# Kernel optimization log

Measured on AMD Instinct MI355X. Metric: run time of the kernel, lower is better.

Reference implementation:

```python
import jax, jax.numpy as jnp
import numpy as np


def _mlp(x, W1, b1, W2, b2):
    # Linear -> exact GELU (torch nn.GELU default) -> Linear
    h = jax.nn.gelu(x @ W1 + b1, approximate=False)
    return h @ W2 + b2


def setup_inputs() -> dict:
    B, L, H, NB, D, HID = 4, 4096, 16, 64, 1024, 128
    NS = H * NB
    key = jax.random.key(0)
    ks = jax.random.split(key, 6)
    theta_path = jax.random.normal(ks[0], (B, L, H, NB), dtype=jnp.float32)
    content_emb = jax.random.normal(ks[1], (B, L, D), dtype=jnp.float32)
    log_Pi = jnp.zeros((H, NB), dtype=jnp.float32)
    s1 = 1.0 / np.sqrt(D)
    s2 = 1.0 / np.sqrt(HID)
    # log_R_head: Linear(D,128) -> GELU -> Linear(128,NS), last weight scaled by 0.01, bias 0
    Wr1 = jax.random.uniform(ks[2], (D, HID), jnp.float32, -s1, s1)
    br1 = jnp.zeros((HID,), jnp.float32)
    Wr2 = jax.random.uniform(ks[3], (HID, NS), jnp.float32, -s2, s2) * 0.01
    br2 = jnp.zeros((NS,), jnp.float32)
    # measure_head: Linear(D,128) -> GELU -> Linear(128,NS)
    Wm1 = jax.random.uniform(ks[4], (D, HID), jnp.float32, -s1, s1)
    bm1 = jnp.zeros((HID,), jnp.float32)
    Wm2 = jax.random.uniform(ks[5], (HID, NS), jnp.float32, -s2, s2)
    bm2 = jnp.zeros((NS,), jnp.float32)
    return {
        "theta_path": theta_path, "content_emb": content_emb, "log_Pi": log_Pi,
        "Wr1": Wr1, "br1": br1, "Wr2": Wr2, "br2": br2,
        "Wm1": Wm1, "bm1": bm1, "Wm2": Wm2, "bm2": bm2,
    }


def reference(theta_path, content_emb, log_Pi, Wr1, br1, Wr2, br2, Wm1, bm1, Wm2, bm2):
    B, L, H, NB = theta_path.shape
    # per-token measurement noise R_t
    log_R = jnp.clip(_mlp(content_emb, Wr1, br1, Wr2, br2).reshape(B, L, H, NB), -5.0, 5.0)
    R = jnp.exp(log_R)
    # measurement z in (-pi, pi)
    z = jnp.pi * jnp.tanh(_mlp(content_emb, Wm1, bm1, Wm2, bm2).reshape(B, L, H, NB))
    diff = z - theta_path
    nu = jnp.arctan2(jnp.sin(diff), jnp.cos(diff))  # wrapped innovation
    Pi = jnp.exp(log_Pi)            # (H, NB) constant covariance
    Pi_b = Pi[None, None]           # (1,1,H,NB)
    K = Pi_b / jnp.maximum(Pi_b + R, 1e-8)  # Kalman gain
    alpha = 1.0 - K
    u = K * nu
    # scalar affine parallel scan: d[t] = alpha[t]*d[t-1] + u[t], d[-1]=0
    def combine(c1, c2):
        a1, v1 = c1
        a2, v2 = c2
        return a1 * a2, a2 * v1 + v2
    _, d = jax.lax.associative_scan(combine, (alpha, u), axis=1)
    theta_hat = theta_path + d
    return theta_hat, Pi, K, R
```

## Files before the change

kernel.cpp:

```cpp
#include <hip/hip_runtime.h>
#include <math.h>

static constexpr size_t OUT_THETA = 0;
static constexpr size_t OUT_PI    = 16777216;
static constexpr size_t OUT_K     = 16778240;
static constexpr size_t OUT_R     = 33555456;

#define PI_F     3.14159265358979323846f
#define INV2PI_F 0.15915494309189535f
#define PI2_HI   6.28318548202514648f
#define PI2_LO  -1.7484556e-7f
#define SPLIT_S  2048.0f
#define SPLIT_IS (1.0f / 2048.0f)

typedef _Float16 half8 __attribute__((ext_vector_type(8)));
typedef float    f32x4 __attribute__((ext_vector_type(4)));

__device__ __forceinline__ float gelu_f(float x) {
    return 0.5f * x * (1.0f + erff(x * 0.70710678118654752f));
}

__global__ __launch_bounds__(256) void k_prep(
    const float* __restrict__ Wr1, const float* __restrict__ Wm1,
    const float* __restrict__ Wr2, const float* __restrict__ Wm2,
    _Float16* __restrict__ W1rT, _Float16* __restrict__ W1mTh, _Float16* __restrict__ W1mTl,
    _Float16* __restrict__ W2rT, _Float16* __restrict__ W2mTh, _Float16* __restrict__ W2mTl)
{
    const int i = blockIdx.x * 256 + threadIdx.x;
    {
        const int k = i >> 7, c = i & 127;
        const int o = c * 1024 + k;
        W1rT[o] = (_Float16)Wr1[i];
        float w = Wm1[i];
        _Float16 h = (_Float16)w;
        W1mTh[o] = h;
        W1mTl[o] = (_Float16)((w - (float)h) * SPLIT_S);
    }
    {
        const int k = i >> 10, c = i & 1023;
        const int o = c * 128 + k;
        W2rT[o] = (_Float16)Wr2[i];
        float w = Wm2[i];
        _Float16 h = (_Float16)w;
        W2mTh[o] = h;
        W2mTl[o] = (_Float16)((w - (float)h) * SPLIT_S);
    }
}

template<bool M>
__global__ __launch_bounds__(256, 3) void k_mm1(
    const float* __restrict__ X,
    const _Float16* __restrict__ WTh, const _Float16* __restrict__ WTl,
    const float* __restrict__ bias,
    _Float16* __restrict__ Oh, _Float16* __restrict__ Ol)
{
    __shared__ _Float16 sm[15360];
    _Float16* XH = sm;
    _Float16* XL = sm + 2560;
    _Float16* WH = sm + 5120;
    _Float16* WL = sm + 10240;

    const int m0   = blockIdx.x * 64;
    const int tid  = threadIdx.x;
    const int lane = tid & 63;
    const int quad = lane >> 4, l15 = lane & 15;
    const int rt   = tid >> 6;
    const int arow = tid >> 2, aseg = tid & 3;

    f32x4 accA[8] = {};
    f32x4 accB[8] = {};

    for (int k0 = 0; k0 < 1024; k0 += 32) {
        const float* xp = X + (size_t)(m0 + arow) * 1024 + k0 + aseg * 8;
        float4 xa = *(const float4*)(xp);
        float4 xb = *(const float4*)(xp + 4);
        half8 wh[2], wl[2];
#pragma unroll
        for (int it = 0; it < 2; ++it) {
            const int u = tid + it * 256;
            const int col = u >> 2, ws = u & 3;
            const size_t go = (size_t)col * 1024 + k0 + ws * 8;
            wh[it] = *(const half8*)(WTh + go);
            if (M) wl[it] = *(const half8*)(WTl + go);
        }
        __syncthreads();
        {
            half8 hh, hl;
#pragma unroll
            for (int c = 0; c < 8; ++c) {
                float v = (c < 4) ? ((const float*)&xa)[c] : ((const float*)&xb)[c - 4];
                _Float16 h = (_Float16)v;
                hh[c] = h;
                hl[c] = (_Float16)((v - (float)h) * SPLIT_S);
            }
            *(half8*)&XH[arow * 40 + aseg * 8] = hh;
            *(half8*)&XL[arow * 40 + aseg * 8] = hl;
        }
#pragma unroll
        for (int it = 0; it < 2; ++it) {
            const int u = tid + it * 256;
            const int col = u >> 2, ws = u & 3;
            *(half8*)&WH[col * 40 + ws * 8] = wh[it];
            if (M) *(half8*)&WL[col * 40 + ws * 8] = wl[it];
        }
        __syncthreads();
        half8 ah = *(const half8*)&XH[(rt * 16 + l15) * 40 + quad * 8];
        half8 al;
        if (M) al = *(const half8*)&XL[(rt * 16 + l15) * 40 + quad * 8];
#pragma unroll
        for (int ct = 0; ct < 8; ++ct) {
            half8 bh = *(const half8*)&WH[(ct * 16 + l15) * 40 + quad * 8];
            accA[ct] = __builtin_amdgcn_mfma_f32_16x16x32_f16(ah, bh, accA[ct], 0, 0, 0);
            if (M) {
                half8 bl = *(const half8*)&WL[(ct * 16 + l15) * 40 + quad * 8];
                accB[ct] = __builtin_amdgcn_mfma_f32_16x16x32_f16(ah, bl, accB[ct], 0, 0, 0);
                accB[ct] = __builtin_amdgcn_mfma_f32_16x16x32_f16(al, bh, accB[ct], 0, 0, 0);
            }
        }
    }
#pragma unroll
    for (int ct = 0; ct < 8; ++ct) {
        const int col = ct * 16 + l15;
        const float b = bias[col];
#pragma unroll
        for (int reg = 0; reg < 4; ++reg) {
            const int token = m0 + rt * 16 + quad * 4 + reg;
            float pre = accA[ct][reg] + (M ? accB[ct][reg] * SPLIT_IS : 0.0f) + b;
            float g = gelu_f(pre);
            const size_t o = (size_t)token * 128 + col;
            if (M) {
                _Float16 h = (_Float16)g;
                Oh[o] = h;
                Ol[o] = (_Float16)((g - (float)h) * SPLIT_S);
            } else {
                Oh[o] = (_Float16)g;
            }
        }
    }
}

__global__ __launch_bounds__(256, 2) void k_mm2(
    const _Float16* __restrict__ Hr, const _Float16* __restrict__ Hmh, const _Float16* __restrict__ Hml,
    const _Float16* __restrict__ W2rT, const _Float16* __restrict__ W2mTh, const _Float16* __restrict__ W2mTl,
    const float* __restrict__ br2, const float* __restrict__ bm2,
    const float* __restrict__ log_Pi, const float* __restrict__ theta,
    float* __restrict__ out, float* __restrict__ Aws, float* __restrict__ Uws)
{
    __shared__ _Float16 sm[30720];
    _Float16* AHr = sm;
    _Float16* AHm = sm + 10240;
    _Float16* ALm = sm + 20480;

    const int tt = blockIdx.x;
    const int jt = blockIdx.y;
    const int m0 = tt * 64, n0 = jt * 64;
    const int tid  = threadIdx.x;
    const int lane = tid & 63;
    const int quad = lane >> 4, l15 = lane & 15;
    const int ct   = tid >> 6;
    const int row  = tid >> 2, seg = tid & 3;

    half8 brf[4], bmf[4], blf[4];
    {
        const size_t bbase = (size_t)(n0 + ct * 16 + l15) * 128 + quad * 8;
#pragma unroll
        for (int k = 0; k < 4; ++k) {
            brf[k] = *(const half8*)(W2rT  + bbase + k * 32);
            bmf[k] = *(const half8*)(W2mTh + bbase + k * 32);
            blf[k] = *(const half8*)(W2mTl + bbase + k * 32);
        }
    }

    {
        const size_t abase = (size_t)(m0 + row) * 128 + seg * 8;
#pragma unroll
        for (int k = 0; k < 4; ++k) {
            half8 la = *(const half8*)(Hr  + abase + k * 32);
            half8 lb = *(const half8*)(Hmh + abase + k * 32);
            half8 lc = *(const half8*)(Hml + abase + k * 32);
            const int so = k * 2560 + row * 40 + seg * 8;
            *(half8*)&AHr[so] = la;
            *(half8*)&AHm[so] = lb;
            *(half8*)&ALm[so] = lc;
        }
    }
    __syncthreads();

    f32x4 accr[4] = {};
    f32x4 accA[4] = {};
    f32x4 accB[4] = {};
#pragma unroll
    for (int k = 0; k < 4; ++k) {
#pragma unroll
        for (int rt = 0; rt < 4; ++rt) {
            const int aidx = k * 2560 + (rt * 16 + l15) * 40 + quad * 8;
            half8 a_r = *(const half8*)&AHr[aidx];
            half8 a_h = *(const half8*)&AHm[aidx];
            half8 a_l = *(const half8*)&ALm[aidx];
            accr[rt] = __builtin_amdgcn_mfma_f32_16x16x32_f16(a_r, brf[k], accr[rt], 0, 0, 0);
            accA[rt] = __builtin_amdgcn_mfma_f32_16x16x32_f16(a_h, bmf[k], accA[rt], 0, 0, 0);
            accB[rt] = __builtin_amdgcn_mfma_f32_16x16x32_f16(a_h, blf[k], accB[rt], 0, 0, 0);
            accB[rt] = __builtin_amdgcn_mfma_f32_16x16x32_f16(a_l, bmf[k], accB[rt], 0, 0, 0);
        }
    }

    const int col = n0 + ct * 16 + l15;
    const float Pi_  = expf(log_Pi[col]);
    const float b2rv = br2[col];
    const float b2mv = bm2[col];
    float segA[4], segU[4];
#pragma unroll
    for (int rt = 0; rt < 4; ++rt) {
        float A = 1.0f, U = 0.0f;
#pragma unroll
        for (int reg = 0; reg < 4; ++reg) {
            const int token = m0 + rt * 16 + quad * 4 + reg;
            const size_t idx = (size_t)token * 1024 + col;
            float lr = fminf(fmaxf(accr[rt][reg] + b2rv, -5.0f), 5.0f);
            float R  = expf(lr);
            float Kg = __fdividef(Pi_, fmaxf(Pi_ + R, 1e-8f));
            float zp = accA[rt][reg] + accB[rt][reg] * SPLIT_IS + b2mv;
            float z  = PI_F * tanhf(zp);
            float d  = z - theta[idx];
            float n  = rintf(d * INV2PI_F);
            float nu = fmaf(-n, PI2_HI, d);
            nu       = fmaf(-n, PI2_LO, nu);
            float u  = Kg * nu;
            float al = 1.0f - Kg;
            U = fmaf(al, U, u);
            A *= al;
            out[OUT_K + idx]     = Kg;
            out[OUT_R + idx]     = R;
            out[OUT_THETA + idx] = u;
        }
        segA[rt] = A; segU[rt] = U;
    }
    __syncthreads();
    float* cA = (float*)sm;
    float* cU = cA + 1088;
    const int colLocal = ct * 16 + l15;
#pragma unroll
    for (int rt = 0; rt < 4; ++rt) {
        cA[colLocal * 17 + rt * 4 + quad] = segA[rt];
        cU[colLocal * 17 + rt * 4 + quad] = segU[rt];
    }
    __syncthreads();
    if (tid < 64) {
        float A = 1.0f, U = 0.0f;
#pragma unroll
        for (int s = 0; s < 16; ++s) {
            float a = cA[tid * 17 + s];
            float u = cU[tid * 17 + s];
            U = fmaf(a, U, u);
            A *= a;
        }
        Aws[(size_t)tt * 1024 + n0 + tid] = A;
        Uws[(size_t)tt * 1024 + n0 + tid] = U;
    }
}

__global__ __launch_bounds__(256) void k_carry(
    const float* __restrict__ Aws, const float* __restrict__ Uws, float* __restrict__ Cws,
    const float* __restrict__ log_Pi, float* __restrict__ out)
{
    const int b = blockIdx.x >> 2;
    const int j = (blockIdx.x & 3) * 256 + threadIdx.x;
    if (blockIdx.x < 4) out[OUT_PI + j] = expf(log_Pi[j]);
    float carry = 0.0f;
    for (int c = 0; c < 64; ++c) {
        const size_t off = (size_t)(b * 64 + c) * 1024 + j;
        float a = Aws[off], u = Uws[off];
        Cws[off] = carry;
        carry = fmaf(a, carry, u);
    }
}

__global__ __launch_bounds__(256) void k_apply(
    const float* __restrict__ theta, const float* __restrict__ Cws, float* __restrict__ out)
{
    const int bid = blockIdx.x;
    const int jg = bid & 3;
    const int c  = (bid >> 2) & 63;
    const int b  = bid >> 8;
    const int j  = jg * 256 + threadIdx.x;
    float d = Cws[(size_t)(b * 64 + c) * 1024 + j];
    size_t idx = (size_t)(b * 4096 + c * 64) * 1024 + j;
    const float* __restrict__ Kbase = out + OUT_K;
#pragma unroll 4
    for (int i = 0; i < 64; ++i) {
        float Kg = Kbase[idx];
        float u  = out[idx];
        d = fmaf(1.0f - Kg, d, u);
        out[idx] = theta[idx] + d;
        idx += 1024;
    }
}

extern "C" void kernel_launch(void* const* d_in, const int* in_sizes, int n_in,
                              void* d_out, int out_size, void* d_ws, size_t ws_size,
                              hipStream_t stream)
{
    const float* theta = (const float*)d_in[0];
    const float* x     = (const float*)d_in[1];
    const float* logPi = (const float*)d_in[2];
    const float* Wr1   = (const float*)d_in[3];
    const float* br1   = (const float*)d_in[4];
    const float* Wr2   = (const float*)d_in[5];
    const float* br2   = (const float*)d_in[6];
    const float* Wm1   = (const float*)d_in[7];
    const float* bm1   = (const float*)d_in[8];
    const float* Wm2   = (const float*)d_in[9];
    const float* bm2   = (const float*)d_in[10];
    float* out = (float*)d_out;

    _Float16* Hr    = (_Float16*)d_ws;
    _Float16* Hmh   = Hr  + (size_t)16384 * 128;
    _Float16* Hml   = Hmh + (size_t)16384 * 128;
    _Float16* W1rT  = Hml + (size_t)16384 * 128;
    _Float16* W1mTh = W1rT  + 131072;
    _Float16* W1mTl = W1mTh + 131072;
    _Float16* W2rT  = W1mTl + 131072;
    _Float16* W2mTh = W2rT  + 131072;
    _Float16* W2mTl = W2mTh + 131072;
    float* Aws = (float*)(W2mTl + 131072);
    float* Uws = Aws + 262144;
    float* Cws = Uws + 262144;

    k_prep<<<512, 256, 0, stream>>>(Wr1, Wm1, Wr2, Wm2,
                                    W1rT, W1mTh, W1mTl, W2rT, W2mTh, W2mTl);
    k_mm1<false><<<256, 256, 0, stream>>>(x, W1rT, nullptr, br1, Hr, nullptr);
    k_mm1<true ><<<256, 256, 0, stream>>>(x, W1mTh, W1mTl, bm1, Hmh, Hml);
    k_mm2<<<dim3(256, 16), 256, 0, stream>>>(Hr, Hmh, Hml, W2rT, W2mTh, W2mTl,
                                             br2, bm2, logPi, theta, out, Aws, Uws);
    k_carry<<<16, 256, 0, stream>>>(Aws, Uws, Cws, logPi, out);
    k_apply<<<1024, 256, 0, stream>>>(theta, Cws, out);
}
```

Baseline: 527.9 us.

## Drop LDS staging in both GEMM kernels, load MFMA fragments directly from global

Both matmul kernels stop staging the A and B tiles in shared memory and instead load MFMA operand fragments straight from global memory (through the caches) into registers. This removes the LDS writes and reads and the __syncthreads barriers in the k-loop, and launch bounds are raised to four blocks per CU to improve occupancy. The cost is uncoalesced, strided global loads: each lane reads 16 bytes from a different row. Operands reused across waves in a block are now fetched repeatedly from L1/L2 instead of once into LDS, and loads are no longer double-buffered or prefetched.

```diff
diff --git a/kernel.cpp b/kernel.cpp
--- a/kernel.cpp
+++ b/kernel.cpp
@@ -48,71 +48,41 @@
 }
 
 template<bool M>
-__global__ __launch_bounds__(256, 3) void k_mm1(
+__global__ __launch_bounds__(256, 4) void k_mm1(
     const float* __restrict__ X,
     const _Float16* __restrict__ WTh, const _Float16* __restrict__ WTl,
     const float* __restrict__ bias,
     _Float16* __restrict__ Oh, _Float16* __restrict__ Ol)
 {
-    __shared__ _Float16 sm[15360];
-    _Float16* XH = sm;
-    _Float16* XL = sm + 2560;
-    _Float16* WH = sm + 5120;
-    _Float16* WL = sm + 10240;
-
     const int m0   = blockIdx.x * 64;
     const int tid  = threadIdx.x;
     const int lane = tid & 63;
     const int quad = lane >> 4, l15 = lane & 15;
     const int rt   = tid >> 6;
-    const int arow = tid >> 2, aseg = tid & 3;
 
     f32x4 accA[8] = {};
     f32x4 accB[8] = {};
 
+    const float* xp = X + (size_t)(m0 + rt * 16 + l15) * 1024 + quad * 8;
+
     for (int k0 = 0; k0 < 1024; k0 += 32) {
-        const float* xp = X + (size_t)(m0 + arow) * 1024 + k0 + aseg * 8;
-        float4 xa = *(const float4*)(xp);
-        float4 xb = *(const float4*)(xp + 4);
-        half8 wh[2], wl[2];
-#pragma unroll
-        for (int it = 0; it < 2; ++it) {
-            const int u = tid + it * 256;
-            const int col = u >> 2, ws = u & 3;
-            const size_t go = (size_t)col * 1024 + k0 + ws * 8;
-            wh[it] = *(const half8*)(WTh + go);
-            if (M) wl[it] = *(const half8*)(WTl + go);
-        }
-        __syncthreads();
-        {
-            half8 hh, hl;
-#pragma unroll
-            for (int c = 0; c < 8; ++c) {
-                float v = (c < 4) ? ((const float*)&xa)[c] : ((const float*)&xb)[c - 4];
-                _Float16 h = (_Float16)v;
-                hh[c] = h;
-                hl[c] = (_Float16)((v - (float)h) * SPLIT_S);
-            }
-            *(half8*)&XH[arow * 40 + aseg * 8] = hh;
-            *(half8*)&XL[arow * 40 + aseg * 8] = hl;
-        }
-#pragma unroll
-        for (int it = 0; it < 2; ++it) {
-            const int u = tid + it * 256;
-            const int col = u >> 2, ws = u & 3;
-            *(half8*)&WH[col * 40 + ws * 8] = wh[it];
-            if (M) *(half8*)&WL[col * 40 + ws * 8] = wl[it];
-        }
-        __syncthreads();
-        half8 ah = *(const half8*)&XH[(rt * 16 + l15) * 40 + quad * 8];
-        half8 al;
-        if (M) al = *(const half8*)&XL[(rt * 16 + l15) * 40 + quad * 8];
+        float4 xa = *(const float4*)(xp + k0);
+        float4 xb = *(const float4*)(xp + k0 + 4);
+        half8 ah, al;
+#pragma unroll
+        for (int c = 0; c < 8; ++c) {
+            float v = (c < 4) ? ((const float*)&xa)[c] : ((const float*)&xb)[c - 4];
+            _Float16 h = (_Float16)v;
+            ah[c] = h;
+            if (M) al[c] = (_Float16)((v - (float)h) * SPLIT_S);
+        }
 #pragma unroll
         for (int ct = 0; ct < 8; ++ct) {
-            half8 bh = *(const half8*)&WH[(ct * 16 + l15) * 40 + quad * 8];
+            const size_t wo = (size_t)(ct * 16 + l15) * 1024 + k0 + quad * 8;
+            half8 bh = *(const half8*)(WTh + wo);
             accA[ct] = __builtin_amdgcn_mfma_f32_16x16x32_f16(ah, bh, accA[ct], 0, 0, 0);
             if (M) {
-                half8 bl = *(const half8*)&WL[(ct * 16 + l15) * 40 + quad * 8];
+                half8 bl = *(const half8*)(WTl + wo);
                 accB[ct] = __builtin_amdgcn_mfma_f32_16x16x32_f16(ah, bl, accB[ct], 0, 0, 0);
                 accB[ct] = __builtin_amdgcn_mfma_f32_16x16x32_f16(al, bh, accB[ct], 0, 0, 0);
             }
@@ -139,17 +109,14 @@
     }
 }
 
-__global__ __launch_bounds__(256, 2) void k_mm2(
+__global__ __launch_bounds__(256, 4) void k_mm2(
     const _Float16* __restrict__ Hr, const _Float16* __restrict__ Hmh, const _Float16* __restrict__ Hml,
     const _Float16* __restrict__ W2rT, const _Float16* __restrict__ W2mTh, const _Float16* __restrict__ W2mTl,
     const float* __restrict__ br2, const float* __restrict__ bm2,
     const float* __restrict__ log_Pi, const float* __restrict__ theta,
     float* __restrict__ out, float* __restrict__ Aws, float* __restrict__ Uws)
 {
-    __shared__ _Float16 sm[30720];
-    _Float16* AHr = sm;
-    _Float16* AHm = sm + 10240;
-    _Float16* ALm = sm + 20480;
+    __shared__ float cAU[2176];
 
     const int tt = blockIdx.x;
     const int jt = blockIdx.y;
@@ -158,49 +125,27 @@
     const int lane = tid & 63;
     const int quad = lane >> 4, l15 = lane & 15;
     const int ct   = tid >> 6;
-    const int row  = tid >> 2, seg = tid & 3;
-
-    half8 brf[4], bmf[4], blf[4];
-    {
-        const size_t bbase = (size_t)(n0 + ct * 16 + l15) * 128 + quad * 8;
-#pragma unroll
-        for (int k = 0; k < 4; ++k) {
-            brf[k] = *(const half8*)(W2rT  + bbase + k * 32);
-            bmf[k] = *(const half8*)(W2mTh + bbase + k * 32);
-            blf[k] = *(const half8*)(W2mTl + bbase + k * 32);
-        }
-    }
-
-    {
-        const size_t abase = (size_t)(m0 + row) * 128 + seg * 8;
-#pragma unroll
-        for (int k = 0; k < 4; ++k) {
-            half8 la = *(const half8*)(Hr  + abase + k * 32);
-            half8 lb = *(const half8*)(Hmh + abase + k * 32);
-            half8 lc = *(const half8*)(Hml + abase + k * 32);
-            const int so = k * 2560 + row * 40 + seg * 8;
-            *(half8*)&AHr[so] = la;
-            *(half8*)&AHm[so] = lb;
-            *(half8*)&ALm[so] = lc;
-        }
-    }
-    __syncthreads();
 
     f32x4 accr[4] = {};
     f32x4 accA[4] = {};
     f32x4 accB[4] = {};
+
+    const size_t bbase = (size_t)(n0 + ct * 16 + l15) * 128 + quad * 8;
 #pragma unroll
     for (int k = 0; k < 4; ++k) {
+        half8 br_ = *(const half8*)(W2rT  + bbase + k * 32);
+        half8 bm_ = *(const half8*)(W2mTh + bbase + k * 32);
+        half8 bl_ = *(const half8*)(W2mTl + bbase + k * 32);
 #pragma unroll
         for (int rt = 0; rt < 4; ++rt) {
-            const int aidx = k * 2560 + (rt * 16 + l15) * 40 + quad * 8;
-            half8 a_r = *(const half8*)&AHr[aidx];
-            half8 a_h = *(const half8*)&AHm[aidx];
-            half8 a_l = *(const half8*)&ALm[aidx];
-            accr[rt] = __builtin_amdgcn_mfma_f32_16x16x32_f16(a_r, brf[k], accr[rt], 0, 0, 0);
-            accA[rt] = __builtin_amdgcn_mfma_f32_16x16x32_f16(a_h, bmf[k], accA[rt], 0, 0, 0);
-            accB[rt] = __builtin_amdgcn_mfma_f32_16x16x32_f16(a_h, blf[k], accB[rt], 0, 0, 0);
-            accB[rt] = __builtin_amdgcn_mfma_f32_16x16x32_f16(a_l, bmf[k], accB[rt], 0, 0, 0);
+            const size_t ao = (size_t)(m0 + rt * 16 + l15) * 128 + k * 32 + quad * 8;
+            half8 a_r = *(const half8*)(Hr  + ao);
+            half8 a_h = *(const half8*)(Hmh + ao);
+            half8 a_l = *(const half8*)(Hml + ao);
+            accr[rt] = __builtin_amdgcn_mfma_f32_16x16x32_f16(a_r, br_, accr[rt], 0, 0, 0);
+            accA[rt] = __builtin_amdgcn_mfma_f32_16x16x32_f16(a_h, bm_, accA[rt], 0, 0, 0);
+            accB[rt] = __builtin_amdgcn_mfma_f32_16x16x32_f16(a_h, bl_, accB[rt], 0, 0, 0);
+            accB[rt] = __builtin_amdgcn_mfma_f32_16x16x32_f16(a_l, bm_, accB[rt], 0, 0, 0);
         }
     }
 
@@ -235,9 +180,8 @@
         }
         segA[rt] = A; segU[rt] = U;
     }
-    __syncthreads();
-    float* cA = (float*)sm;
-    float* cU = cA + 1088;
+    float* cA = cAU;
+    float* cU = cAU + 1088;
     const int colLocal = ct * 16 + l15;
 #pragma unroll
     for (int rt = 0; rt < 4; ++rt) {
```

New measurement: 628.0 us. +19.0%, slower.

## Fuse both first-layer MLP GEMMs into one kernel and K-tile second GEMM

Applied to the files above, without the earlier changes.

The two first-layer GEMM launches (log_R head and measure head) are merged into one kernel, so each block converts and stages the shared content_emb tile once and reads x from memory once instead of twice. The second GEMM kernel now streams K in 32-wide chunks through smaller shared-memory tiles for both A and B, and its occupancy hint rises from 2 to 4 blocks. This cuts LDS per block and register-held B fragments. In exchange, the fused mm1 holds more accumulators, which raises register pressure at 3 blocks per CU, and mm2 now has extra barriers per K step.

```diff
diff --git a/kernel.cpp b/kernel.cpp
--- a/kernel.cpp
+++ b/kernel.cpp
@@ -47,18 +47,19 @@
     }
 }
 
-template<bool M>
 __global__ __launch_bounds__(256, 3) void k_mm1(
     const float* __restrict__ X,
-    const _Float16* __restrict__ WTh, const _Float16* __restrict__ WTl,
-    const float* __restrict__ bias,
-    _Float16* __restrict__ Oh, _Float16* __restrict__ Ol)
-{
-    __shared__ _Float16 sm[15360];
+    const _Float16* __restrict__ WrT,
+    const _Float16* __restrict__ WmTh, const _Float16* __restrict__ WmTl,
+    const float* __restrict__ br1, const float* __restrict__ bm1,
+    _Float16* __restrict__ OHr, _Float16* __restrict__ OHmh, _Float16* __restrict__ OHml)
+{
+    __shared__ _Float16 sm[20480];
     _Float16* XH = sm;
     _Float16* XL = sm + 2560;
-    _Float16* WH = sm + 5120;
-    _Float16* WL = sm + 10240;
+    _Float16* WR = sm + 5120;
+    _Float16* WH = sm + 10240;
+    _Float16* WL = sm + 15360;
 
     const int m0   = blockIdx.x * 64;
     const int tid  = threadIdx.x;
@@ -67,6 +68,7 @@
     const int rt   = tid >> 6;
     const int arow = tid >> 2, aseg = tid & 3;
 
+    f32x4 accR[8] = {};
     f32x4 accA[8] = {};
     f32x4 accB[8] = {};
 
@@ -74,14 +76,15 @@
         const float* xp = X + (size_t)(m0 + arow) * 1024 + k0 + aseg * 8;
         float4 xa = *(const float4*)(xp);
         float4 xb = *(const float4*)(xp + 4);
-        half8 wh[2], wl[2];
+        half8 wr[2], wh[2], wl[2];
 #pragma unroll
         for (int it = 0; it < 2; ++it) {
             const int u = tid + it * 256;
             const int col = u >> 2, ws = u & 3;
             const size_t go = (size_t)col * 1024 + k0 + ws * 8;
-            wh[it] = *(const half8*)(WTh + go);
-            if (M) wl[it] = *(const half8*)(WTl + go);
+            wr[it] = *(const half8*)(WrT  + go);
+            wh[it] = *(const half8*)(WmTh + go);
+            wl[it] = *(const half8*)(WmTl + go);
         }
         __syncthreads();
         {
@@ -100,56 +103,57 @@
         for (int it = 0; it < 2; ++it) {
             const int u = tid + it * 256;
             const int col = u >> 2, ws = u & 3;
+            *(half8*)&WR[col * 40 + ws * 8] = wr[it];
             *(half8*)&WH[col * 40 + ws * 8] = wh[it];
-            if (M) *(half8*)&WL[col * 40 + ws * 8] = wl[it];
+            *(half8*)&WL[col * 40 + ws * 8] = wl[it];
         }
         __syncthreads();
         half8 ah = *(const half8*)&XH[(rt * 16 + l15) * 40 + quad * 8];
-        half8 al;
-        if (M) al = *(const half8*)&XL[(rt * 16 + l15) * 40 + quad * 8];
+        half8 al = *(const half8*)&XL[(rt * 16 + l15) * 40 + quad * 8];
 #pragma unroll
         for (int ct = 0; ct < 8; ++ct) {
-            half8 bh = *(const half8*)&WH[(ct * 16 + l15) * 40 + quad * 8];
-            accA[ct] = __builtin_amdgcn_mfma_f32_16x16x32_f16(ah, bh, accA[ct], 0, 0, 0);
-            if (M) {
-                half8 bl = *(const half8*)&WL[(ct * 16 + l15) * 40 + quad * 8];
-                accB[ct] = __builtin_amdgcn_mfma_f32_16x16x32_f16(ah, bl, accB[ct], 0, 0, 0);
-                accB[ct] = __builtin_amdgcn_mfma_f32_16x16x32_f16(al, bh, accB[ct], 0, 0, 0);
-            }
+            half8 bhr = *(const half8*)&WR[(ct * 16 + l15) * 40 + quad * 8];
+            accR[ct] = __builtin_amdgcn_mfma_f32_16x16x32_f16(ah, bhr, accR[ct], 0, 0, 0);
+            half8 bhm = *(const half8*)&WH[(ct * 16 + l15) * 40 + quad * 8];
+            accA[ct] = __builtin_amdgcn_mfma_f32_16x16x32_f16(ah, bhm, accA[ct], 0, 0, 0);
+            half8 blm = *(const half8*)&WL[(ct * 16 + l15) * 40 + quad * 8];
+            accB[ct] = __builtin_amdgcn_mfma_f32_16x16x32_f16(ah, blm, accB[ct], 0, 0, 0);
+            accB[ct] = __builtin_amdgcn_mfma_f32_16x16x32_f16(al, bhm, accB[ct], 0, 0, 0);
         }
     }
 #pragma unroll
     for (int ct = 0; ct < 8; ++ct) {
         const int col = ct * 16 + l15;
-        const float b = bias[col];
+        const float bR = br1[col];
+        const float bM = bm1[col];
 #pragma unroll
         for (int reg = 0; reg < 4; ++reg) {
             const int token = m0 + rt * 16 + quad * 4 + reg;
-            float pre = accA[ct][reg] + (M ? accB[ct][reg] * SPLIT_IS : 0.0f) + b;
-            float g = gelu_f(pre);
             const size_t o = (size_t)token * 128 + col;
-            if (M) {
-                _Float16 h = (_Float16)g;
-                Oh[o] = h;
-                Ol[o] = (_Float16)((g - (float)h) * SPLIT_S);
-            } else {
-                Oh[o] = (_Float16)g;
-            }
-        }
-    }
-}
-
-__global__ __launch_bounds__(256, 2) void k_mm2(
+            float gr = gelu_f(accR[ct][reg] + bR);
+            OHr[o] = (_Float16)gr;
+            float gm = gelu_f(accA[ct][reg] + accB[ct][reg] * SPLIT_IS + bM);
+            _Float16 h = (_Float16)gm;
+            OHmh[o] = h;
+            OHml[o] = (_Float16)((gm - (float)h) * SPLIT_S);
+        }
+    }
+}
+
+__global__ __launch_bounds__(256, 4) void k_mm2(
     const _Float16* __restrict__ Hr, const _Float16* __restrict__ Hmh, const _Float16* __restrict__ Hml,
     const _Float16* __restrict__ W2rT, const _Float16* __restrict__ W2mTh, const _Float16* __restrict__ W2mTl,
     const float* __restrict__ br2, const float* __restrict__ bm2,
     const float* __restrict__ log_Pi, const float* __restrict__ theta,
     float* __restrict__ out, float* __restrict__ Aws, float* __restrict__ Uws)
 {
-    __shared__ _Float16 sm[30720];
+    __shared__ _Float16 sm[15360];
     _Float16* AHr = sm;
-    _Float16* AHm = sm + 10240;
-    _Float16* ALm = sm + 20480;
+    _Float16* AHm = sm + 2560;
+    _Float16* ALm = sm + 5120;
+    _Float16* BHr = sm + 7680;
+    _Float16* BHm = sm + 10240;
+    _Float16* BLm = sm + 12800;
 
     const int tt = blockIdx.x;
     const int jt = blockIdx.y;
@@ -160,47 +164,42 @@
     const int ct   = tid >> 6;
     const int row  = tid >> 2, seg = tid & 3;
 
-    half8 brf[4], bmf[4], blf[4];
-    {
-        const size_t bbase = (size_t)(n0 + ct * 16 + l15) * 128 + quad * 8;
-#pragma unroll
-        for (int k = 0; k < 4; ++k) {
-            brf[k] = *(const half8*)(W2rT  + bbase + k * 32);
-            bmf[k] = *(const half8*)(W2mTh + bbase + k * 32);
-            blf[k] = *(const half8*)(W2mTl + bbase + k * 32);
-        }
-    }
-
-    {
-        const size_t abase = (size_t)(m0 + row) * 128 + seg * 8;
-#pragma unroll
-        for (int k = 0; k < 4; ++k) {
-            half8 la = *(const half8*)(Hr  + abase + k * 32);
-            half8 lb = *(const half8*)(Hmh + abase + k * 32);
-            half8 lc = *(const half8*)(Hml + abase + k * 32);
-            const int so = k * 2560 + row * 40 + seg * 8;
-            *(half8*)&AHr[so] = la;
-            *(half8*)&AHm[so] = lb;
-            *(half8*)&ALm[so] = lc;
-        }
-    }
-    __syncthreads();
-
     f32x4 accr[4] = {};
     f32x4 accA[4] = {};
     f32x4 accB[4] = {};
-#pragma unroll
-    for (int k = 0; k < 4; ++k) {
+
+    for (int k0 = 0; k0 < 128; k0 += 32) {
+        const size_t ao = (size_t)(m0 + row) * 128 + k0 + seg * 8;
+        const size_t bo = (size_t)(n0 + row) * 128 + k0 + seg * 8;
+        half8 la = *(const half8*)(Hr  + ao);
+        half8 lb = *(const half8*)(Hmh + ao);
+        half8 lc = *(const half8*)(Hml + ao);
+        half8 ld = *(const half8*)(W2rT  + bo);
+        half8 le = *(const half8*)(W2mTh + bo);
+        half8 lf = *(const half8*)(W2mTl + bo);
+        __syncthreads();
+        const int so = row * 40 + seg * 8;
+        *(half8*)&AHr[so] = la;
+        *(half8*)&AHm[so] = lb;
+        *(half8*)&ALm[so] = lc;
+        *(half8*)&BHr[so] = ld;
+        *(half8*)&BHm[so] = le;
+        *(half8*)&BLm[so] = lf;
+        __syncthreads();
+        const int bidx = (ct * 16 + l15) * 40 + quad * 8;
+        half8 br_ = *(const half8*)&BHr[bidx];
+        half8 bm_ = *(const half8*)&BHm[bidx];
+        half8 bl_ = *(const half8*)&BLm[bidx];
 #pragma unroll
         for (int rt = 0; rt < 4; ++rt) {
-            const int aidx = k * 2560 + (rt * 16 + l15) * 40 + quad * 8;
+            const int aidx = (rt * 16 + l15) * 40 + quad * 8;
             half8 a_r = *(const half8*)&AHr[aidx];
             half8 a_h = *(const half8*)&AHm[aidx];
             half8 a_l = *(const half8*)&ALm[aidx];
-            accr[rt] = __builtin_amdgcn_mfma_f32_16x16x32_f16(a_r, brf[k], accr[rt], 0, 0, 0);
-            accA[rt] = __builtin_amdgcn_mfma_f32_16x16x32_f16(a_h, bmf[k], accA[rt], 0, 0, 0);
-            accB[rt] = __builtin_amdgcn_mfma_f32_16x16x32_f16(a_h, blf[k], accB[rt], 0, 0, 0);
-            accB[rt] = __builtin_amdgcn_mfma_f32_16x16x32_f16(a_l, bmf[k], accB[rt], 0, 0, 0);
+            accr[rt] = __builtin_amdgcn_mfma_f32_16x16x32_f16(a_r, br_, accr[rt], 0, 0, 0);
+            accA[rt] = __builtin_amdgcn_mfma_f32_16x16x32_f16(a_h, bm_, accA[rt], 0, 0, 0);
+            accB[rt] = __builtin_amdgcn_mfma_f32_16x16x32_f16(a_h, bl_, accB[rt], 0, 0, 0);
+            accB[rt] = __builtin_amdgcn_mfma_f32_16x16x32_f16(a_l, bm_, accB[rt], 0, 0, 0);
         }
     }
 
@@ -328,8 +327,7 @@
 
     k_prep<<<512, 256, 0, stream>>>(Wr1, Wm1, Wr2, Wm2,
                                     W1rT, W1mTh, W1mTl, W2rT, W2mTh, W2mTl);
-    k_mm1<false><<<256, 256, 0, stream>>>(x, W1rT, nullptr, br1, Hr, nullptr);
-    k_mm1<true ><<<256, 256, 0, stream>>>(x, W1mTh, W1mTl, bm1, Hmh, Hml);
+    k_mm1<<<256, 256, 0, stream>>>(x, W1rT, W1mTh, W1mTl, br1, bm1, Hr, Hmh, Hml);
     k_mm2<<<dim3(256, 16), 256, 0, stream>>>(Hr, Hmh, Hml, W2rT, W2mTh, W2mTl,
                                              br2, bm2, logPi, theta, out, Aws, Uws);
     k_carry<<<16, 256, 0, stream>>>(Aws, Uws, Cws, logPi, out);
```

Result: faster. 474.6 us (-10.1%).
